# Kernel optimization log

Measured on AMD Instinct MI355X. Metric: run time of the kernel, lower is better.

Reference implementation:

```python
import jax, jax.numpy as jnp
import numpy as np

N = 131072          # total sampled proposals (flattened over batch)
D = 1024            # num_extractor_out
C = 21              # num_classes (VOC: 20 + background)


def setup_inputs() -> dict:
    key = jax.random.key(0)
    k1, k2, k3 = jax.random.split(key, 3)
    features = jax.random.normal(k1, (N, D), dtype=jnp.float32)
    # Linear weights stored as [in, out] so y = x @ W + b
    W_cls = jax.random.normal(k2, (D, C), dtype=jnp.float32) * (1.0 / np.sqrt(D))
    b_cls = jnp.zeros((C,), dtype=jnp.float32)
    W_tf = jax.random.normal(k3, (D, C * 4), dtype=jnp.float32) * (1.0 / np.sqrt(D))
    b_tf = jnp.zeros((C * 4,), dtype=jnp.float32)
    return {"features": features, "W_cls": W_cls, "b_cls": b_cls, "W_tf": W_tf, "b_tf": b_tf}


def reference(features, W_cls, b_cls, W_tf, b_tf):
    # ROI.forward with identity extractor / no pre/post transforms.
    proposal_classes = features @ W_cls + b_cls                    # [N, C]
    proposal_transformers = features @ W_tf + b_tf                 # [N, C*4]
    proposal_transformers = proposal_transformers.reshape(features.shape[0], C, 4)
    return proposal_classes, proposal_transformers
```

## Files before the change

kernel.cpp:

```cpp
#include <hip/hip_runtime.h>
#include <hip/hip_bf16.h>

#define NROWS 131072
#define DK    1024
#define CCLS  21
#define CTF   84
#define NCOL  105
#define NCT   7
#define BM    16
#define SLABF 128
#define NSLAB (DK / SLABF)

typedef __attribute__((ext_vector_type(4))) float f32x4;
typedef __attribute__((ext_vector_type(8))) short bf16x8;
typedef __attribute__((ext_vector_type(2))) unsigned int u32x2;

__device__ __forceinline__ unsigned short f2bf_rne(float x) {
    union { float f; unsigned u; } v; v.f = x;
    unsigned r = v.u + 0x7fffu + ((v.u >> 16) & 1u);
    return (unsigned short)(r >> 16);
}

__device__ __forceinline__ unsigned pack2(float lo, float hi) {
    union { float f; unsigned u; } a, b; a.f = lo; b.f = hi;
    return ((a.u + 0x8000u) >> 16) | ((b.u + 0x8000u) & 0xffff0000u);
}

__global__ void pack_B_kernel(const float* __restrict__ Wc,
                              const float* __restrict__ Wt,
                              unsigned short* __restrict__ Bp) {
    const int frag = blockIdx.x;
    const int kt = frag / NCT, ct = frag % NCT;
    const int lane = threadIdx.x;
    const int col = ct * 16 + (lane & 15);
    const int k0  = kt * 32 + ((lane >> 4) << 3);
    bf16x8 o;
#pragma unroll
    for (int j = 0; j < 8; ++j) {
        const int k = k0 + j;
        float v = 0.0f;
        if (col < CCLS)      v = Wc[k * CCLS + col];
        else if (col < NCOL) v = Wt[k * CTF + (col - CCLS)];
        o[j] = (short)f2bf_rne(v);
    }
    *reinterpret_cast<bf16x8*>(Bp + ((size_t)frag * 64 + lane) * 8) = o;
}

__global__ __launch_bounds__(256, 4)
void roi_gemm_kernel(const float* __restrict__ F,
                     const unsigned short* __restrict__ Bp,
                     const float* __restrict__ bcls,
                     const float* __restrict__ btf,
                     float* __restrict__ out) {
    __shared__ __align__(16) unsigned char smem[28672];

    const int t    = threadIdx.x;
    const int wave = t >> 6;
    const int lane = t & 63;
    const int fr   = lane & 15;
    const int fq   = lane >> 4;
    const long rw  = (long)blockIdx.x * BM;

    const unsigned short* bb = Bp + (size_t)lane * 8;
    const float* asrc = F + (size_t)(rw + wave * 4 + (lane >> 5)) * DK
                        + (lane & 31) * 4;

    const int c   = (lane & 31) >> 1;
    const int h8  = (lane & 1) << 3;
    const int R0  = wave * 4 + (lane >> 5);
    const int R1  = R0 + 2;
    const int w0  = R0 * 256 + (((c) ^ (R0 & 7)) << 4) + h8;
    const int w1  = R1 * 256 + (((c) ^ (R1 & 7)) << 4) + h8;
    const int rdoff = fr * 256 + (((wave * 4 + fq) ^ (fr & 7)) << 4);

    f32x4 acc[NCT];
#pragma unroll
    for (int ct = 0; ct < NCT; ++ct) acc[ct] = (f32x4){0.f, 0.f, 0.f, 0.f};

    f32x4 vP[2], vQ[2];
    bf16x8 bfrP[NCT], bfrQ[NCT];

#define LOADA(V, S) do {                                                      \
    V[0] = *reinterpret_cast<const f32x4*>(asrc + (size_t)(S) * SLABF);       \
    V[1] = *reinterpret_cast<const f32x4*>(asrc + (size_t)(S) * SLABF         \
                                           + 2 * DK);                         \
} while (0)

#define LOADB(BF, S) do {                                                     \
    const int ktg_ = (S) * 4 + wave;                                          \
    _Pragma("unroll")                                                         \
    for (int ct = 0; ct < NCT; ++ct)                                          \
        BF[ct] = *reinterpret_cast<const bf16x8*>(                            \
            bb + ((size_t)(ktg_ * NCT + ct) * 512));                          \
} while (0)

#define WRITEA(V, BUF) do {                                                   \
    u32x2 d0_; d0_[0] = pack2(V[0][0], V[0][1]);                              \
    d0_[1] = pack2(V[0][2], V[0][3]);                                         \
    u32x2 d1_; d1_[0] = pack2(V[1][0], V[1][1]);                              \
    d1_[1] = pack2(V[1][2], V[1][3]);                                         \
    *reinterpret_cast<u32x2*>(smem + (BUF) * 4096 + w0) = d0_;                \
    *reinterpret_cast<u32x2*>(smem + (BUF) * 4096 + w1) = d1_;                \
} while (0)

#define COMPUTE(BF, BUF) do {                                                 \
    const bf16x8 a_ = *reinterpret_cast<const bf16x8*>(                       \
        smem + (BUF) * 4096 + rdoff);                                         \
    _Pragma("unroll")                                                         \
    for (int ct = 0; ct < NCT; ++ct)                                          \
        acc[ct] = __builtin_amdgcn_mfma_f32_16x16x32_bf16(                    \
            a_, BF[ct], acc[ct], 0, 0, 0);                                    \
} while (0)

#define SLAB(S, BCUR, BNXT, VW, VL) do {                                      \
    if ((S) + 1 < NSLAB) LOADB(BNXT, (S) + 1);                                \
    __builtin_amdgcn_sched_barrier(0);                                        \
    if ((S) + 2 < NSLAB) LOADA(VL, (S) + 2);                                  \
    __builtin_amdgcn_sched_barrier(0);                                        \
    COMPUTE(BCUR, (S) & 1);                                                   \
    __builtin_amdgcn_sched_barrier(0);                                        \
    if ((S) + 1 < NSLAB) {                                                    \
        WRITEA(VW, ((S) + 1) & 1);                                            \
        __builtin_amdgcn_sched_barrier(0);                                    \
        asm volatile("s_waitcnt lgkmcnt(0)" ::: "memory");                    \
        __builtin_amdgcn_s_barrier();                                         \
        __builtin_amdgcn_sched_barrier(0);                                    \
    }                                                                         \
} while (0)

    LOADA(vP, 0);
    LOADA(vQ, 1);
    LOADB(bfrP, 0);
    __builtin_amdgcn_sched_barrier(0);
    WRITEA(vP, 0);
    __builtin_amdgcn_sched_barrier(0);
    asm volatile("s_waitcnt lgkmcnt(0)" ::: "memory");
    __builtin_amdgcn_s_barrier();
    __builtin_amdgcn_sched_barrier(0);

    SLAB(0, bfrP, bfrQ, vQ, vP);
    SLAB(1, bfrQ, bfrP, vP, vQ);
    SLAB(2, bfrP, bfrQ, vQ, vP);
    SLAB(3, bfrQ, bfrP, vP, vQ);
    SLAB(4, bfrP, bfrQ, vQ, vP);
    SLAB(5, bfrQ, bfrP, vP, vQ);
    SLAB(6, bfrP, bfrQ, vQ, vP);
    SLAB(7, bfrQ, bfrP, vP, vQ);

#undef SLAB
#undef COMPUTE
#undef WRITEA
#undef LOADB
#undef LOADA

    __syncthreads();
    float* sf = reinterpret_cast<float*>(smem);
#pragma unroll
    for (int ct = 0; ct < NCT; ++ct)
        *reinterpret_cast<f32x4*>(sf + ((wave * NCT + ct) << 8) + (lane << 2)) =
            acc[ct];
    __syncthreads();

    const int rcol0 = (t >> 2) & 15;
    float* out_tf = out + (size_t)NROWS * CCLS;
    const long grow = rw + ((t >> 6) << 2) + (t & 3);
#pragma unroll
    for (int ct = 0; ct < NCT; ++ct) {
        const int col = ct * 16 + rcol0;
        if (col >= NCOL) continue;
        const float v = sf[(0 * NCT + ct) * 256 + t] +
                        sf[(1 * NCT + ct) * 256 + t] +
                        sf[(2 * NCT + ct) * 256 + t] +
                        sf[(3 * NCT + ct) * 256 + t] +
                        ((col < CCLS) ? bcls[col] : btf[col - CCLS]);
        if (col < CCLS) out[grow * CCLS + col] = v;
        else            out_tf[grow * CTF + (col - CCLS)] = v;
    }
}

extern "C" void kernel_launch(void* const* d_in, const int* in_sizes, int n_in,
                              void* d_out, int out_size, void* d_ws, size_t ws_size,
                              hipStream_t stream) {
    const float* F  = (const float*)d_in[0];
    const float* Wc = (const float*)d_in[1];
    const float* bc = (const float*)d_in[2];
    const float* Wt = (const float*)d_in[3];
    const float* bt = (const float*)d_in[4];
    unsigned short* Bp = (unsigned short*)d_ws;

    pack_B_kernel<<<NCT * (DK / 32), 64, 0, stream>>>(Wc, Wt, Bp);
    roi_gemm_kernel<<<NROWS / BM, 256, 0, stream>>>(F, Bp, bc, bt,
                                                    (float*)d_out);
}
```

Baseline: 162.1 us.

## Widen K slab to 256 and drop B-fragment double buffering

Each pipeline step now covers 256 K columns instead of 128. Each wave loads four rows of A per slab, and the A tile in shared memory holds 512-byte rows, double buffered. Every wave handles two K-tiles of 32 per slab, so the number of barrier-separated steps falls from 8 to 4. This cuts per-slab barrier and sync overhead. The B fragments are no longer prefetched one slab ahead; they are loaded at the start of the same slab that uses them, which can expose their latency. The launch-bound occupancy hint drops from 4 to 3 blocks per CU to make room for the larger register footprint.

```diff
diff --git a/kernel.cpp b/kernel.cpp
--- a/kernel.cpp
+++ b/kernel.cpp
@@ -8,7 +8,7 @@
 #define NCOL  105
 #define NCT   7
 #define BM    16
-#define SLABF 128
+#define SLABF 256
 #define NSLAB (DK / SLABF)
 
 typedef __attribute__((ext_vector_type(4))) float f32x4;
@@ -46,7 +46,7 @@
     *reinterpret_cast<bf16x8*>(Bp + ((size_t)frag * 64 + lane) * 8) = o;
 }
 
-__global__ __launch_bounds__(256, 4)
+__global__ __launch_bounds__(256, 3)
 void roi_gemm_kernel(const float* __restrict__ F,
                      const unsigned short* __restrict__ Bp,
                      const float* __restrict__ bcls,
@@ -62,32 +62,26 @@
     const long rw  = (long)blockIdx.x * BM;
 
     const unsigned short* bb = Bp + (size_t)lane * 8;
-    const float* asrc = F + (size_t)(rw + wave * 4 + (lane >> 5)) * DK
-                        + (lane & 31) * 4;
-
-    const int c   = (lane & 31) >> 1;
-    const int h8  = (lane & 1) << 3;
-    const int R0  = wave * 4 + (lane >> 5);
-    const int R1  = R0 + 2;
-    const int w0  = R0 * 256 + (((c) ^ (R0 & 7)) << 4) + h8;
-    const int w1  = R1 * 256 + (((c) ^ (R1 & 7)) << 4) + h8;
-    const int rdoff = fr * 256 + (((wave * 4 + fq) ^ (fr & 7)) << 4);
+    const float* asrc = F + (size_t)(rw + wave * 4) * DK + lane * 4;
 
     f32x4 acc[NCT];
 #pragma unroll
     for (int ct = 0; ct < NCT; ++ct) acc[ct] = (f32x4){0.f, 0.f, 0.f, 0.f};
 
-    f32x4 vP[2], vQ[2];
-    bf16x8 bfrP[NCT], bfrQ[NCT];
+    f32x4 vP[4], vQ[4];
+    bf16x8 bfr0[NCT], bfr1[NCT];
+
+#define SB __builtin_amdgcn_sched_barrier(0)
 
 #define LOADA(V, S) do {                                                      \
-    V[0] = *reinterpret_cast<const f32x4*>(asrc + (size_t)(S) * SLABF);       \
-    V[1] = *reinterpret_cast<const f32x4*>(asrc + (size_t)(S) * SLABF         \
-                                           + 2 * DK);                         \
+    _Pragma("unroll")                                                         \
+    for (int q = 0; q < 4; ++q)                                               \
+        V[q] = *reinterpret_cast<const f32x4*>(                               \
+            asrc + (size_t)q * DK + (size_t)(S) * SLABF);                     \
 } while (0)
 
-#define LOADB(BF, S) do {                                                     \
-    const int ktg_ = (S) * 4 + wave;                                          \
+#define LOADB(BF, S, JJ) do {                                                 \
+    const int ktg_ = (S) * 8 + wave * 2 + (JJ);                               \
     _Pragma("unroll")                                                         \
     for (int ct = 0; ct < NCT; ++ct)                                          \
         BF[ct] = *reinterpret_cast<const bf16x8*>(                            \
@@ -95,63 +89,66 @@
 } while (0)
 
 #define WRITEA(V, BUF) do {                                                   \
-    u32x2 d0_; d0_[0] = pack2(V[0][0], V[0][1]);                              \
-    d0_[1] = pack2(V[0][2], V[0][3]);                                         \
-    u32x2 d1_; d1_[0] = pack2(V[1][0], V[1][1]);                              \
-    d1_[1] = pack2(V[1][2], V[1][3]);                                         \
-    *reinterpret_cast<u32x2*>(smem + (BUF) * 4096 + w0) = d0_;                \
-    *reinterpret_cast<u32x2*>(smem + (BUF) * 4096 + w1) = d1_;                \
+    _Pragma("unroll")                                                         \
+    for (int q = 0; q < 4; ++q) {                                             \
+        const int R_ = wave * 4 + q;                                          \
+        u32x2 d_;                                                             \
+        d_[0] = pack2(V[q][0], V[q][1]);                                      \
+        d_[1] = pack2(V[q][2], V[q][3]);                                      \
+        *reinterpret_cast<u32x2*>(smem + (BUF) * 8192 + R_ * 512 +            \
+            (((lane >> 1) ^ (R_ & 7)) << 4) + ((lane & 1) << 3)) = d_;        \
+    }                                                                         \
 } while (0)
 
-#define COMPUTE(BF, BUF) do {                                                 \
+#define COMPUTE(BF, BUF, JJ) do {                                             \
+    const int lt_ = wave * 2 + (JJ);                                          \
     const bf16x8 a_ = *reinterpret_cast<const bf16x8*>(                       \
-        smem + (BUF) * 4096 + rdoff);                                         \
+        smem + (BUF) * 8192 + fr * 512 +                                      \
+        ((((lt_ << 2) | fq) ^ (fr & 7)) << 4));                               \
     _Pragma("unroll")                                                         \
     for (int ct = 0; ct < NCT; ++ct)                                          \
         acc[ct] = __builtin_amdgcn_mfma_f32_16x16x32_bf16(                    \
             a_, BF[ct], acc[ct], 0, 0, 0);                                    \
 } while (0)
 
-#define SLAB(S, BCUR, BNXT, VW, VL) do {                                      \
-    if ((S) + 1 < NSLAB) LOADB(BNXT, (S) + 1);                                \
-    __builtin_amdgcn_sched_barrier(0);                                        \
-    if ((S) + 2 < NSLAB) LOADA(VL, (S) + 2);                                  \
-    __builtin_amdgcn_sched_barrier(0);                                        \
-    COMPUTE(BCUR, (S) & 1);                                                   \
-    __builtin_amdgcn_sched_barrier(0);                                        \
+#define SLAB(S, VL, VW) do {                                                  \
+    LOADB(bfr0, S, 0);                                                        \
+    LOADB(bfr1, S, 1);                                                        \
+    SB;                                                                       \
+    if ((S) + 2 < NSLAB) { LOADA(VL, (S) + 2); }                              \
+    SB;                                                                       \
+    COMPUTE(bfr0, (S) & 1, 0);                                                \
+    COMPUTE(bfr1, (S) & 1, 1);                                                \
+    SB;                                                                       \
     if ((S) + 1 < NSLAB) {                                                    \
         WRITEA(VW, ((S) + 1) & 1);                                            \
-        __builtin_amdgcn_sched_barrier(0);                                    \
+        SB;                                                                   \
         asm volatile("s_waitcnt lgkmcnt(0)" ::: "memory");                    \
         __builtin_amdgcn_s_barrier();                                         \
-        __builtin_amdgcn_sched_barrier(0);                                    \
+        SB;                                                                   \
     }                                                                         \
 } while (0)
 
     LOADA(vP, 0);
     LOADA(vQ, 1);
-    LOADB(bfrP, 0);
-    __builtin_amdgcn_sched_barrier(0);
+    SB;
     WRITEA(vP, 0);
-    __builtin_amdgcn_sched_barrier(0);
+    SB;
     asm volatile("s_waitcnt lgkmcnt(0)" ::: "memory");
     __builtin_amdgcn_s_barrier();
-    __builtin_amdgcn_sched_barrier(0);
+    SB;
 
-    SLAB(0, bfrP, bfrQ, vQ, vP);
-    SLAB(1, bfrQ, bfrP, vP, vQ);
-    SLAB(2, bfrP, bfrQ, vQ, vP);
-    SLAB(3, bfrQ, bfrP, vP, vQ);
-    SLAB(4, bfrP, bfrQ, vQ, vP);
-    SLAB(5, bfrQ, bfrP, vP, vQ);
-    SLAB(6, bfrP, bfrQ, vQ, vP);
-    SLAB(7, bfrQ, bfrP, vP, vQ);
+    SLAB(0, vP, vQ);
+    SLAB(1, vQ, vP);
+    SLAB(2, vP, vQ);
+    SLAB(3, vP, vQ);
 
 #undef SLAB
 #undef COMPUTE
 #undef WRITEA
 #undef LOADB
 #undef LOADA
+#undef SB
 
     __syncthreads();
     float* sf = reinterpret_cast<float*>(smem);
```

Result: faster. 151.8 us (-6.4%).
